# Kernel tuning notes

Hardware: AMD Instinct MI355X
Metric: run time of the kernel (lower is better)

The kernel has to match this reference:

```python
import jax, jax.numpy as jnp
import numpy as np


def _2div(arr):
    arr_res = arr.copy()
    arr_pieces = []
    pa = 0
    st = 0
    needdivcnt = 0
    for i, a in enumerate(arr):
        if a != pa:
            arr_pieces.append([st, i])
            if i - st != 1:
                needdivcnt += 1
            pa = a
            st = i
    arr_pieces.append([st, len(arr)])
    if len(arr) - st != 1:
        needdivcnt += 1
    offset = range(len(arr_pieces), len(arr_pieces) + needdivcnt)
    p = 0
    for arr_p in arr_pieces:
        length = arr_p[1] - arr_p[0]
        if length == 1:
            continue
        half_len = int(np.ceil(length / 2))
        for j in range(arr_p[0] + half_len, arr_p[1]):
            arr_res[j] = offset[p]
        p += 1
    return arr_res


def get_division_tree(n_agents):
    agent2divitreeindex = np.arange(n_agents)
    np.random.shuffle(agent2divitreeindex)
    max_div = np.ceil(np.log2(n_agents)).astype(int)
    levels = np.zeros(shape=(max_div + 1, n_agents), dtype=int)
    for ith in range(1, len(levels)):
        levels[ith, :] = _2div(levels[ith - 1, :])
    res_levels = levels.copy()
    for i, idx in enumerate(agent2divitreeindex):
        res_levels[:, i] = levels[:, idx]
    return res_levels


def setup_inputs() -> dict:
    B, A, H, NACT = 2048, 50, 512, 64
    F = H + A  # in-features of first Linear (hidden + one-hot agent id)
    np.random.seed(0)
    div_tree = get_division_tree(A)
    routing = jnp.asarray(div_tree[-1], dtype=jnp.int32)  # max_level routing: agent -> net index
    key = jax.random.key(0)
    k0, k1, k2 = jax.random.split(key, 3)
    x_in = jax.random.normal(k0, (B, A, H), dtype=jnp.float32)
    # stacked per-net parameters (n_nets == n_agent independent 2-layer MLPs)
    W1 = jax.random.normal(k1, (A, F, H), dtype=jnp.float32) * (1.0 / np.sqrt(F))
    b1 = jnp.zeros((A, H), dtype=jnp.float32)
    W2 = jax.random.normal(k2, (A, H, NACT), dtype=jnp.float32) * (1.0 / np.sqrt(H))
    b2 = jnp.zeros((A, NACT), dtype=jnp.float32)
    return {"x_in": x_in, "W1": W1, "b1": b1, "W2": W2, "b2": b2, "routing": routing}


def reference(x_in, W1, b1, W2, b2, routing):
    # x_in: [B, A, H]; routing: [A] int (which net each agent uses)
    B, A, H = x_in.shape
    # add_onehot_id_at_last_dim: append agent-id one-hot -> [B, A, H+A]
    onehot = jnp.broadcast_to(jnp.eye(A, dtype=x_in.dtype), (B, A, A))
    x0 = jnp.concatenate([x_in, onehot], axis=-1)
    # gather routed expert weights per agent
    W1r, b1r = W1[routing], b1[routing]   # [A, H+A, H], [A, H]
    W2r, b2r = W2[routing], b2[routing]   # [A, H, NACT], [A, NACT]
    h = jax.nn.relu(jnp.einsum('baf,afh->bah', x0, W1r) + b1r)
    out = jnp.einsum('bah,ahn->ban', h, W2r) + b2r  # [B, A, NACT]
    return out
```

## Files before the change

### kernel.cpp

```cpp
#include <hip/hip_runtime.h>

typedef __attribute__((ext_vector_type(8))) short bf16x8;
typedef __attribute__((ext_vector_type(4))) float f32x4;
typedef __attribute__((ext_vector_type(4))) unsigned short u16x4;

#define B_ 2048
#define A_ 50
#define H_ 512
#define NACT_ 64
#define F_ 562
#define BM_ 64
#define BK_ 32
#define NSTEP_ (H_ / BK_)

#define WS_W1T 0
#define WS_W2T ((size_t)A_ * H_ * H_ * 2)
#define WS_B1 (WS_W2T + (size_t)A_ * NACT_ * H_ * 2)
#define WS_B2 (WS_B1 + (size_t)A_ * H_ * 4)

static __device__ __forceinline__ unsigned short f2bf(float f) {
  unsigned int u = __builtin_bit_cast(unsigned int, f);
  u += 0x7fffu + ((u >> 16) & 1u);
  return (unsigned short)(u >> 16);
}

static __device__ __forceinline__ void gld_lds16(const unsigned short* src,
                                                 unsigned short* dst) {
  __builtin_amdgcn_global_load_lds(
      (const __attribute__((address_space(1))) unsigned int*)(const void*)src,
      (__attribute__((address_space(3))) unsigned int*)(void*)dst, 16, 0, 0);
}

static __device__ __forceinline__ int clamp_r(int r) {
  return r < 0 ? 0 : (r > A_ - 1 ? A_ - 1 : r);
}

__global__ void prep_w1(const float* __restrict__ w1,
                        const int* __restrict__ routing,
                        unsigned short* __restrict__ w1t) {
  const int bid = blockIdx.x;
  const int a = bid / 64;
  const int tile = bid - a * 64;
  const int tk = tile & 7, tj = tile >> 3;
  const int k0 = tk * 64, j0 = tj * 64;
  const int r = clamp_r(routing[a]);
  __shared__ float tl[64][65];
  const int t = threadIdx.x;
  const int c = t & 63, q = t >> 6;
#pragma unroll
  for (int i = 0; i < 16; ++i) {
    const int kl = q + i * 4;
    tl[kl][c] = w1[((size_t)r * F_ + k0 + kl) * H_ + j0 + c];
  }
  __syncthreads();
#pragma unroll
  for (int i = 0; i < 16; ++i) {
    const int jl = q + i * 4;
    const int j = j0 + jl;
    const int k = k0 + c;
    const int ts = k >> 5;
    const int sub = (k >> 3) & 3;
    const int elem = k & 7;
    const size_t idx = (((size_t)a * 16 + ts) * H_ + j) * 32 +
                       (size_t)((sub ^ (j & 3)) * 8 + elem);
    w1t[idx] = f2bf(tl[c][jl]);
  }
}

__global__ void prep_w2(const float* __restrict__ w2,
                        const int* __restrict__ routing,
                        unsigned short* __restrict__ w2t) {
  const int bid = blockIdx.x;
  const int a = bid >> 3;
  const int tk = bid & 7;
  const int k0 = tk * 64;
  const int r = clamp_r(routing[a]);
  __shared__ float tl[64][65];
  const int t = threadIdx.x;
  const int c = t & 63, q = t >> 6;
#pragma unroll
  for (int i = 0; i < 16; ++i) {
    const int kl = q + i * 4;
    tl[kl][c] = w2[((size_t)r * H_ + k0 + kl) * NACT_ + c];
  }
  __syncthreads();
#pragma unroll
  for (int i = 0; i < 16; ++i) {
    const int nl = q + i * 4;
    w2t[((size_t)a * NACT_ + nl) * H_ + k0 + c] = f2bf(tl[c][nl]);
  }
}

__global__ void prep_bias(const float* __restrict__ w1,
                          const float* __restrict__ b1,
                          const float* __restrict__ b2,
                          const int* __restrict__ routing,
                          float* __restrict__ bias1, float* __restrict__ bias2) {
  const int a = blockIdx.x;
  const int t = threadIdx.x;
  const int r = clamp_r(routing[a]);
  bias1[a * H_ + t] = b1[(size_t)r * H_ + t] + w1[((size_t)r * F_ + H_ + a) * H_ + t];
  if (t < NACT_) bias2[a * NACT_ + t] = b2[r * NACT_ + t];
}

__global__ __launch_bounds__(512, 4) void divtree_main(
    const float* __restrict__ x, const unsigned short* __restrict__ w1t,
    const unsigned short* __restrict__ w2t, const float* __restrict__ bias1,
    const float* __restrict__ bias2, float* __restrict__ out) {
  __shared__ union {
    struct {
      unsigned short w1[2][H_ * BK_];
      unsigned short xs[2][BM_ * BK_];
    } st;
    unsigned short h[BM_ * H_];
  } sm;

  const int bid = blockIdx.x;
  const int swz = (bid & 7) * 200 + (bid >> 3);
  const int a = swz >> 5;
  const int mblk = swz & 31;
  const int b0 = mblk * BM_;

  const int tid = threadIdx.x;
  const int lane = tid & 63;
  const int w = tid >> 6;
  const int l16 = lane & 15;
  const int lk = lane >> 4;
  const int sxor = lk ^ (l16 & 3);

  const int wj = w * 64;

  const unsigned short* w1ta = w1t + (size_t)a * (H_ * H_);

  const int xrow = tid >> 3;
  const int xq = tid & 7;
  const float* xbase =
      x + ((size_t)(b0 + xrow) * A_ + (size_t)a) * H_ + (size_t)xq * 4;
  const int xs_off = xrow * BK_ + ((xq >> 1) ^ (xrow & 3)) * 8 + (xq & 1) * 4;

  const int afr_base = (wj + l16) * BK_ + sxor * 8;
  const int bfr_base = l16 * BK_ + sxor * 8;

  f32x4 acc[4][4];
#pragma unroll
  for (int i = 0; i < 4; ++i)
#pragma unroll
    for (int j = 0; j < 4; ++j) acc[i][j] = (f32x4){0.f, 0.f, 0.f, 0.f};

  f32x4 xv;

  {
    xv = *(const f32x4*)(xbase);
#pragma unroll
    for (int i = 0; i < 4; ++i) {
      const unsigned short* src = w1ta + ((size_t)(i * 512 + tid) << 3);
      unsigned short* dst = sm.st.w1[0] + (size_t)(i * 512 + (w << 6)) * 8;
      gld_lds16(src, dst);
    }
    u16x4 v;
#pragma unroll
    for (int e = 0; e < 4; ++e) v[e] = f2bf(xv[e]);
    *(u16x4*)(sm.st.xs[0] + xs_off) = v;
  }
  __syncthreads();

  int cur = 0;
  for (int t = 0; t < NSTEP_; ++t) {
    const bool pf = (t + 1 < NSTEP_);
    if (pf) {
      xv = *(const f32x4*)(xbase + (t + 1) * BK_);
      const unsigned short* wsrc = w1ta + (size_t)(t + 1) * (H_ * BK_);
#pragma unroll
      for (int i = 0; i < 4; ++i) {
        const unsigned short* src = wsrc + ((size_t)(i * 512 + tid) << 3);
        unsigned short* dst =
            sm.st.w1[cur ^ 1] + (size_t)(i * 512 + (w << 6)) * 8;
        gld_lds16(src, dst);
      }
    }
    const unsigned short* w1s = sm.st.w1[cur];
    const unsigned short* xss = sm.st.xs[cur];
    bf16x8 afr[4], bfr[4];
#pragma unroll
    for (int jf = 0; jf < 4; ++jf)
      afr[jf] = *(const bf16x8*)(w1s + afr_base + jf * (16 * BK_));
#pragma unroll
    for (int mf = 0; mf < 4; ++mf)
      bfr[mf] = *(const bf16x8*)(xss + bfr_base + mf * (16 * BK_));
#pragma unroll
    for (int jf = 0; jf < 4; ++jf)
#pragma unroll
      for (int mf = 0; mf < 4; ++mf)
        acc[jf][mf] = __builtin_amdgcn_mfma_f32_16x16x32_bf16(
            afr[jf], bfr[mf], acc[jf][mf], 0, 0, 0);
    if (pf) {
      u16x4 v;
#pragma unroll
      for (int e = 0; e < 4; ++e) v[e] = f2bf(xv[e]);
      *(u16x4*)(sm.st.xs[cur ^ 1] + xs_off) = v;
    }
    __syncthreads();
    cur ^= 1;
  }

  const float* b1p = bias1 + a * H_;
#pragma unroll
  for (int jf = 0; jf < 4; ++jf) {
    const f32x4 bv = *(const f32x4*)(b1p + wj + jf * 16 + lk * 4);
    const int cbase = (wj >> 3) + jf * 2 + (lk >> 1);
    const int half4 = (lk & 1) * 4;
#pragma unroll
    for (int mf = 0; mf < 4; ++mf) {
      u16x4 hv;
#pragma unroll
      for (int r = 0; r < 4; ++r) {
        float f = acc[jf][mf][r] + bv[r];
        f = f > 0.f ? f : 0.f;
        hv[r] = f2bf(f);
      }
      const int m = mf * 16 + l16;
      const int off = m * H_ + (cbase ^ (l16 & 7)) * 8 + half4;
      *(u16x4*)(sm.h + off) = hv;
    }
  }
  __syncthreads();

  const int m0 = (w & 1) * 32;
  const int n0 = (w >> 1) * 16;
  const unsigned short* w2p =
      w2t + ((size_t)a * NACT_ + n0 + l16) * H_ + lk * 8;
  f32x4 acc2[2];
  acc2[0] = (f32x4){0.f, 0.f, 0.f, 0.f};
  acc2[1] = (f32x4){0.f, 0.f, 0.f, 0.f};
#pragma unroll
  for (int kf = 0; kf < 16; ++kf) {
    const bf16x8 bf2 = *(const bf16x8*)(w2p + kf * 32);
#pragma unroll
    for (int mf = 0; mf < 2; ++mf) {
      const int row = m0 + mf * 16 + l16;
      const int off = row * H_ + (((kf * 4 + lk) ^ (l16 & 7))) * 8;
      const bf16x8 af2 = *(const bf16x8*)(sm.h + off);
      acc2[mf] = __builtin_amdgcn_mfma_f32_16x16x32_bf16(af2, bf2, acc2[mf],
                                                         0, 0, 0);
    }
  }
  const float b2v = bias2[a * NACT_ + n0 + l16];
#pragma unroll
  for (int mf = 0; mf < 2; ++mf)
#pragma unroll
    for (int r = 0; r < 4; ++r) {
      const int m = m0 + mf * 16 + lk * 4 + r;
      out[((size_t)(b0 + m) * A_ + a) * NACT_ + n0 + l16] = acc2[mf][r] + b2v;
    }
}

extern "C" void kernel_launch(void* const* d_in, const int* in_sizes, int n_in,
                              void* d_out, int out_size, void* d_ws,
                              size_t ws_size, hipStream_t stream) {
  const float* x = (const float*)d_in[0];
  const float* w1 = (const float*)d_in[1];
  const float* b1 = (const float*)d_in[2];
  const float* w2 = (const float*)d_in[3];
  const float* b2 = (const float*)d_in[4];
  const int* routing = (const int*)d_in[5];
  float* out = (float*)d_out;

  char* ws = (char*)d_ws;
  unsigned short* w1t = (unsigned short*)(ws + WS_W1T);
  unsigned short* w2t = (unsigned short*)(ws + WS_W2T);
  float* bias1 = (float*)(ws + WS_B1);
  float* bias2 = (float*)(ws + WS_B2);

  prep_w1<<<A_ * 64, 256, 0, stream>>>(w1, routing, w1t);
  prep_w2<<<A_ * 8, 256, 0, stream>>>(w2, routing, w2t);
  prep_bias<<<A_, 512, 0, stream>>>(w1, b1, b2, routing, bias1, bias2);
  divtree_main<<<A_ * (B_ / BM_), 512, 0, stream>>>(x, w1t, w2t, bias1, bias2,
                                                    out);
}
```

Before: 153.2 us.

## Coalesce x loads in wide batches, stage output through LDS, vectorize W1 prep

The main kernel now loads x as full 512-byte row segments four K-steps at a time. Each lane converts its slice to bf16 once and writes it into the LDS staging buffer on the matching step, which replaces the per-step 128-byte strided loads. The output tile is staged through a padded LDS buffer so each row is written with contiguous 16-byte stores instead of scattered 4-byte ones. The W1 prep transpose now packs 8 bf16 values into one 16-byte store, and the main loop is fully unrolled with launch bounds relaxed from 4 to 2 waves per SIMD. The costs are more registers held for prefetched x, an extra barrier and LDS pass in the epilogue, and possibly lower occupancy.

```diff
diff --git a/kernel.cpp b/kernel.cpp
--- a/kernel.cpp
+++ b/kernel.cpp
@@ -3,6 +3,7 @@
 typedef __attribute__((ext_vector_type(8))) short bf16x8;
 typedef __attribute__((ext_vector_type(4))) float f32x4;
 typedef __attribute__((ext_vector_type(4))) unsigned short u16x4;
+typedef __attribute__((ext_vector_type(8))) unsigned short u16x8;
 
 #define B_ 2048
 #define A_ 50
@@ -12,6 +13,7 @@
 #define BM_ 64
 #define BK_ 32
 #define NSTEP_ (H_ / BK_)
+#define AH_ (A_ * H_)
 
 #define WS_W1T 0
 #define WS_W2T ((size_t)A_ * H_ * H_ * 2)
@@ -54,16 +56,17 @@
   }
   __syncthreads();
 #pragma unroll
-  for (int i = 0; i < 16; ++i) {
-    const int jl = q + i * 4;
+  for (int it = 0; it < 2; ++it) {
+    const int item = it * 256 + t;
+    const int jl = item >> 3, kc = item & 7;
     const int j = j0 + jl;
-    const int k = k0 + c;
-    const int ts = k >> 5;
-    const int sub = (k >> 3) & 3;
-    const int elem = k & 7;
-    const size_t idx = (((size_t)a * 16 + ts) * H_ + j) * 32 +
-                       (size_t)((sub ^ (j & 3)) * 8 + elem);
-    w1t[idx] = f2bf(tl[c][jl]);
+    const int ts = (k0 + kc * 8) >> 5;
+    u16x8 v;
+#pragma unroll
+    for (int e = 0; e < 8; ++e) v[e] = f2bf(tl[kc * 8 + e][jl]);
+    unsigned short* dst = w1t + (((size_t)a * 16 + ts) * H_ + j) * 32 +
+                          (size_t)(((kc & 3) ^ (j & 3)) << 3);
+    *(u16x8*)dst = v;
   }
 }
 
@@ -103,7 +106,7 @@
   if (t < NACT_) bias2[a * NACT_ + t] = b2[r * NACT_ + t];
 }
 
-__global__ __launch_bounds__(512, 4) void divtree_main(
+__global__ __launch_bounds__(512, 2) void divtree_main(
     const float* __restrict__ x, const unsigned short* __restrict__ w1t,
     const unsigned short* __restrict__ w2t, const float* __restrict__ bias1,
     const float* __restrict__ bias2, float* __restrict__ out) {
@@ -113,6 +116,7 @@
       unsigned short xs[2][BM_ * BK_];
     } st;
     unsigned short h[BM_ * H_];
+    float outb[BM_][66];
   } sm;
 
   const int bid = blockIdx.x;
@@ -132,11 +136,18 @@
 
   const unsigned short* w1ta = w1t + (size_t)a * (H_ * H_);
 
-  const int xrow = tid >> 3;
-  const int xq = tid & 7;
-  const float* xbase =
-      x + ((size_t)(b0 + xrow) * A_ + (size_t)a) * H_ + (size_t)xq * 4;
-  const int xs_off = xrow * BK_ + ((xq >> 1) ^ (xrow & 3)) * 8 + (xq & 1) * 4;
+  const int r2 = lane >> 5;
+  const int cc = lane & 31;
+  const int xq = cc & 7;
+  const int xact = cc >> 3;
+  const float* xpt =
+      x + ((size_t)(b0 + (w << 3) + r2) * A_ + (size_t)a) * H_ + (size_t)cc * 4;
+  int xs_off[4];
+#pragma unroll
+  for (int i = 0; i < 4; ++i) {
+    const int row = (w << 3) + 2 * i + r2;
+    xs_off[i] = row * BK_ + ((xq >> 1) ^ (row & 3)) * 8 + (xq & 1) * 4;
+  }
 
   const int afr_base = (wj + l16) * BK_ + sxor * 8;
   const int bfr_base = l16 * BK_ + sxor * 8;
@@ -147,60 +158,73 @@
 #pragma unroll
     for (int j = 0; j < 4; ++j) acc[i][j] = (f32x4){0.f, 0.f, 0.f, 0.f};
 
-  f32x4 xv;
+  f32x4 xr[4];
+  u16x4 xbf[4];
 
   {
-    xv = *(const f32x4*)(xbase);
-#pragma unroll
-    for (int i = 0; i < 4; ++i) {
-      const unsigned short* src = w1ta + ((size_t)(i * 512 + tid) << 3);
-      unsigned short* dst = sm.st.w1[0] + (size_t)(i * 512 + (w << 6)) * 8;
-      gld_lds16(src, dst);
-    }
-    u16x4 v;
-#pragma unroll
-    for (int e = 0; e < 4; ++e) v[e] = f2bf(xv[e]);
-    *(u16x4*)(sm.st.xs[0] + xs_off) = v;
-  }
-  __syncthreads();
-
-  int cur = 0;
+#pragma unroll
+    for (int i = 0; i < 4; ++i)
+      xr[i] = *(const f32x4*)(xpt + (size_t)(2 * i) * AH_);
+#pragma unroll
+    for (int i = 0; i < 4; ++i)
+      gld_lds16(w1ta + ((size_t)(i * 512 + tid) << 3),
+                sm.st.w1[0] + (size_t)(i * 512 + (w << 6)) * 8);
+#pragma unroll
+    for (int i = 0; i < 4; ++i)
+#pragma unroll
+      for (int e = 0; e < 4; ++e) xbf[i][e] = f2bf(xr[i][e]);
+    if (xact == 0) {
+#pragma unroll
+      for (int i = 0; i < 4; ++i) *(u16x4*)(sm.st.xs[0] + xs_off[i]) = xbf[i];
+    }
+  }
+  __syncthreads();
+
+#pragma unroll
   for (int t = 0; t < NSTEP_; ++t) {
+    const int buf = t & 1;
     const bool pf = (t + 1 < NSTEP_);
+    if (((t & 3) == 3) && pf) {
+      const float* p = xpt + (size_t)(t + 1) * BK_;
+#pragma unroll
+      for (int i = 0; i < 4; ++i)
+        xr[i] = *(const f32x4*)(p + (size_t)(2 * i) * AH_);
+    }
     if (pf) {
-      xv = *(const f32x4*)(xbase + (t + 1) * BK_);
       const unsigned short* wsrc = w1ta + (size_t)(t + 1) * (H_ * BK_);
 #pragma unroll
-      for (int i = 0; i < 4; ++i) {
-        const unsigned short* src = wsrc + ((size_t)(i * 512 + tid) << 3);
-        unsigned short* dst =
-            sm.st.w1[cur ^ 1] + (size_t)(i * 512 + (w << 6)) * 8;
-        gld_lds16(src, dst);
+      for (int i = 0; i < 4; ++i)
+        gld_lds16(wsrc + ((size_t)(i * 512 + tid) << 3),
+                  sm.st.w1[buf ^ 1] + (size_t)(i * 512 + (w << 6)) * 8);
+    }
+    {
+      const unsigned short* w1s = sm.st.w1[buf];
+      const unsigned short* xss = sm.st.xs[buf];
+      bf16x8 bfr[4];
+#pragma unroll
+      for (int mf = 0; mf < 4; ++mf)
+        bfr[mf] = *(const bf16x8*)(xss + bfr_base + mf * (16 * BK_));
+#pragma unroll
+      for (int jf = 0; jf < 4; ++jf) {
+        const bf16x8 afr = *(const bf16x8*)(w1s + afr_base + jf * (16 * BK_));
+#pragma unroll
+        for (int mf = 0; mf < 4; ++mf)
+          acc[jf][mf] = __builtin_amdgcn_mfma_f32_16x16x32_bf16(
+              afr, bfr[mf], acc[jf][mf], 0, 0, 0);
       }
     }
-    const unsigned short* w1s = sm.st.w1[cur];
-    const unsigned short* xss = sm.st.xs[cur];
-    bf16x8 afr[4], bfr[4];
-#pragma unroll
-    for (int jf = 0; jf < 4; ++jf)
-      afr[jf] = *(const bf16x8*)(w1s + afr_base + jf * (16 * BK_));
-#pragma unroll
-    for (int mf = 0; mf < 4; ++mf)
-      bfr[mf] = *(const bf16x8*)(xss + bfr_base + mf * (16 * BK_));
-#pragma unroll
-    for (int jf = 0; jf < 4; ++jf)
-#pragma unroll
-      for (int mf = 0; mf < 4; ++mf)
-        acc[jf][mf] = __builtin_amdgcn_mfma_f32_16x16x32_bf16(
-            afr[jf], bfr[mf], acc[jf][mf], 0, 0, 0);
-    if (pf) {
-      u16x4 v;
-#pragma unroll
-      for (int e = 0; e < 4; ++e) v[e] = f2bf(xv[e]);
-      *(u16x4*)(sm.st.xs[cur ^ 1] + xs_off) = v;
+    if (((t & 3) == 3) && pf) {
+#pragma unroll
+      for (int i = 0; i < 4; ++i)
+#pragma unroll
+        for (int e = 0; e < 4; ++e) xbf[i][e] = f2bf(xr[i][e]);
+    }
+    if (pf && xact == ((t + 1) & 3)) {
+#pragma unroll
+      for (int i = 0; i < 4; ++i)
+        *(u16x4*)(sm.st.xs[buf ^ 1] + xs_off[i]) = xbf[i];
     }
     __syncthreads();
-    cur ^= 1;
   }
 
   const float* b1p = bias1 + a * H_;
@@ -219,7 +243,7 @@
         hv[r] = f2bf(f);
       }
       const int m = mf * 16 + l16;
-      const int off = m * H_ + (cbase ^ (l16 & 7)) * 8 + half4;
+      const int off = m * H_ + ((cbase ^ (l16 & 7))) * 8 + half4;
       *(u16x4*)(sm.h + off) = hv;
     }
   }
@@ -245,13 +269,23 @@
     }
   }
   const float b2v = bias2[a * NACT_ + n0 + l16];
+  __syncthreads();
 #pragma unroll
   for (int mf = 0; mf < 2; ++mf)
 #pragma unroll
-    for (int r = 0; r < 4; ++r) {
-      const int m = m0 + mf * 16 + lk * 4 + r;
-      out[((size_t)(b0 + m) * A_ + a) * NACT_ + n0 + l16] = acc2[mf][r] + b2v;
-    }
+    for (int r = 0; r < 4; ++r)
+      sm.outb[m0 + mf * 16 + lk * 4 + r][n0 + l16] = acc2[mf][r] + b2v;
+  __syncthreads();
+
+  {
+    const int row = tid >> 3;
+    const int q8 = (tid & 7) * 8;
+    const f32x4 v0 = *(const f32x4*)(&sm.outb[row][q8]);
+    const f32x4 v1 = *(const f32x4*)(&sm.outb[row][q8 + 4]);
+    float* op = out + ((size_t)(b0 + row) * A_ + a) * NACT_ + q8;
+    *(f32x4*)op = v0;
+    *(f32x4*)(op + 4) = v1;
+  }
 }
 
 extern "C" void kernel_launch(void* const* d_in, const int* in_sizes, int n_in,
```

After: 177.1 us. +15.6%, slower.
